# Performance work log

Hardware: AMD Instinct MI355X
Metric: run time of the kernel (lower is better)

## Reference

```python
import jax, jax.numpy as jnp
import numpy as np

NUM_SEQS = 32
NUM_HEADS = 32
NUM_KV_HEADS = 8
HEAD_DIM = 128
BLOCK_SIZE = 16
MAX_BLOCKS = 128          # max_seq_len 2048 / block_size 16
NUM_BLOCKS = NUM_SEQS * MAX_BLOCKS  # 4096
SCALE = 0.08838834764831845  # 1/sqrt(128)


def setup_inputs() -> dict:
    key = jax.random.key(0)
    kq, kk, kv, kkc, kvc, kbt, kcl = jax.random.split(key, 7)
    q = jax.random.normal(kq, (NUM_SEQS, NUM_HEADS, HEAD_DIM), dtype=jnp.float32)
    k = jax.random.normal(kk, (NUM_SEQS, NUM_KV_HEADS, HEAD_DIM), dtype=jnp.float32)
    v = jax.random.normal(kv, (NUM_SEQS, NUM_KV_HEADS, HEAD_DIM), dtype=jnp.float32)
    k_cache = jax.random.normal(kkc, (NUM_BLOCKS, BLOCK_SIZE, NUM_KV_HEADS, HEAD_DIM), dtype=jnp.float32)
    v_cache = jax.random.normal(kvc, (NUM_BLOCKS, BLOCK_SIZE, NUM_KV_HEADS, HEAD_DIM), dtype=jnp.float32)
    # disjoint paged block tables: permutation of all blocks
    block_tables = jax.random.permutation(kbt, NUM_BLOCKS).reshape(NUM_SEQS, MAX_BLOCKS).astype(jnp.int32)
    context_lens = jax.random.randint(kcl, (NUM_SEQS,), 1, MAX_BLOCKS * BLOCK_SIZE, dtype=jnp.int32)
    # slot for the newest token (position context_len-1) of each sequence
    last = context_lens - 1
    blk = jnp.take_along_axis(block_tables, (last // BLOCK_SIZE)[:, None], axis=1)[:, 0]
    slot_mapping = (blk * BLOCK_SIZE + last % BLOCK_SIZE).astype(jnp.int32)
    return {"q": q, "k": k, "v": v, "k_cache": k_cache, "v_cache": v_cache,
            "slot_mapping": slot_mapping, "block_tables": block_tables,
            "context_lens": context_lens}


def reference(q, k, v, k_cache, v_cache, slot_mapping, block_tables, context_lens):
    nb, bs, nkv, hd = k_cache.shape
    s, h, _ = q.shape
    g = h // nkv  # GQA group size
    # 1) scatter-store new k/v into the paged cache at slot_mapping
    kc = k_cache.reshape(nb * bs, nkv, hd).at[slot_mapping].set(k)
    vc = v_cache.reshape(nb * bs, nkv, hd).at[slot_mapping].set(v)
    kc = kc.reshape(nb, bs, nkv, hd)
    vc = vc.reshape(nb, bs, nkv, hd)
    # 2) gather per-sequence KV via block tables: [S, MB, bs, nkv, hd] -> [S, L, nkv, hd]
    max_len = block_tables.shape[1] * bs
    keys = kc[block_tables].reshape(s, max_len, nkv, hd)
    vals = vc[block_tables].reshape(s, max_len, nkv, hd)
    # 3) GQA decode attention with per-sequence length mask
    qg = q.reshape(s, nkv, g, hd)
    scores = jnp.einsum('sngd,slnd->sngl', qg, keys) * SCALE  # [S, nkv, g, L]
    valid = (jnp.arange(max_len, dtype=jnp.int32)[None, :] < context_lens[:, None])
    scores = jnp.where(valid[:, None, None, :], scores, -1e30)
    probs = jax.nn.softmax(scores, axis=-1)
    out = jnp.einsum('sngl,slnd->sngd', probs, vals)
    return out.reshape(s, h, hd)
```

## Files before the change

kernel.cpp:

```cpp
#include <hip/hip_runtime.h>

#define NUM_SEQS   32
#define NUM_HEADS  32
#define NUM_KV     8
#define GQA        4
#define HD         128
#define BS         16
#define MAX_BLOCKS 128
#define PART       256
#define NPARTS     8
#define SLOG2 (0.08838834764831845f * 1.4426950408889634f)


#define LOADKV(I, KA, KB, VA, VB)                                           \
    {                                                                       \
        const int    blk_  = blkreg[(I) >> 2];                              \
        const int    toff_ = (grp + 4 * (I)) & 15;                          \
        const size_t row_  = (((size_t)blk_ * BS + toff_) * NUM_KV + n) * HD; \
        const float4* kr_ = (const float4*)(kcache + row_);                 \
        const float4* vr_ = (const float4*)(vcache + row_);                 \
        KA = kr_[dsub];      KB = kr_[16 + dsub];                           \
        VA = vr_[dsub];      VB = vr_[16 + dsub];                           \
    }

#define QK_PV(KA, KB, VA, VB)                                               \
    {                                                                       \
        float pr[GQA];                                                      \
        _Pragma("unroll")                                                   \
        for (int h = 0; h < GQA; ++h) {                                     \
            float d = KA.x * qa[h].x + KA.y * qa[h].y + KA.z * qa[h].z      \
                    + KA.w * qa[h].w                                        \
                    + KB.x * qb[h].x + KB.y * qb[h].y + KB.z * qb[h].z      \
                    + KB.w * qb[h].w;                                       \
            d += __shfl_xor(d, 1);                                          \
            d += __shfl_xor(d, 2);                                          \
            d += __shfl_xor(d, 4);                                          \
            d += __shfl_xor(d, 8);                                          \
            pr[h] = exp2f(d * SLOG2);                                       \
            l[h] += pr[h];                                                  \
        }                                                                   \
        _Pragma("unroll")                                                   \
        for (int h = 0; h < GQA; ++h) {                                     \
            aa[h].x += pr[h] * VA.x; aa[h].y += pr[h] * VA.y;               \
            aa[h].z += pr[h] * VA.z; aa[h].w += pr[h] * VA.w;               \
            ab[h].x += pr[h] * VB.x; ab[h].y += pr[h] * VB.y;               \
            ab[h].z += pr[h] * VB.z; ab[h].w += pr[h] * VB.w;               \
        }                                                                   \
    }

__global__ __launch_bounds__(256, 4) void paged_attn_part(
    const float* __restrict__ q, const float* __restrict__ knew,
    const float* __restrict__ vnew, const float* __restrict__ kcache,
    const float* __restrict__ vcache, const int* __restrict__ block_tables,
    const int* __restrict__ context_lens,
    float* __restrict__ ws_acc, float* __restrict__ ws_l)
{
    const int p = blockIdx.x;
    const int n = blockIdx.y;
    const int s = blockIdx.z;
    const int L = context_lens[s];
    const int t0 = p * PART;
    if (t0 >= L) return;

    const int tid  = threadIdx.x;
    const int wave = tid >> 6;
    const int lane = tid & 63;
    const int grp  = lane >> 4;
    const int dsub = lane & 15;

    __shared__ int   lds_bt[16];
    __shared__ float lds_acc[4][GQA][HD];
    __shared__ float lds_l[4][GQA];

    if (tid < 16) lds_bt[tid] = block_tables[s * MAX_BLOCKS + (t0 >> 4) + tid];
    __syncthreads();

    int blkreg[4];
#pragma unroll
    for (int j = 0; j < 4; ++j) blkreg[j] = lds_bt[wave * 4 + j];

    float4 qa[GQA], qb[GQA];
#pragma unroll
    for (int h = 0; h < GQA; ++h) {
        const float4* qp = (const float4*)(q + ((size_t)s * NUM_HEADS + n * GQA + h) * HD);
        qa[h] = qp[dsub];
        qb[h] = qp[16 + dsub];
    }

    float l[GQA];
    float4 aa[GQA], ab[GQA];
#pragma unroll
    for (int h = 0; h < GQA; ++h) {
        l[h] = 0.f;
        aa[h] = make_float4(0.f, 0.f, 0.f, 0.f);
        ab[h] = make_float4(0.f, 0.f, 0.f, 0.f);
    }

    const int Leff = L - 1;
    const int ntok = min(Leff - t0, PART);
    int wtok = ntok - wave * 64;
    if (wtok > 64) wtok = 64;
    const int avail = wtok - grp;
    const int nit = (avail > 0) ? ((avail + 3) >> 2) : 0;

    float4 k0a, k0b, v0a, v0b;
    float4 k1a, k1b, v1a, v1b;
    if (nit > 0) LOADKV(0, k0a, k0b, v0a, v0b);
    if (nit > 1) LOADKV(1, k1a, k1b, v1a, v1b);

    int i = 0;
#pragma unroll 1
    for (; i + 2 <= nit; i += 2) {
        QK_PV(k0a, k0b, v0a, v0b);
        if (i + 2 < nit) LOADKV(i + 2, k0a, k0b, v0a, v0b);
        QK_PV(k1a, k1b, v1a, v1b);
        if (i + 3 < nit) LOADKV(i + 3, k1a, k1b, v1a, v1b);
    }
    if (i < nit) QK_PV(k0a, k0b, v0a, v0b);

    if ((t0 >> 8) == ((L - 1) >> 8) && tid < 16) {
        const float4* kr = (const float4*)(knew + ((size_t)s * NUM_KV + n) * HD);
        const float4* vr = (const float4*)(vnew + ((size_t)s * NUM_KV + n) * HD);
        const float4 ka = kr[dsub];
        const float4 kb = kr[16 + dsub];
        const float4 va = vr[dsub];
        const float4 vb = vr[16 + dsub];
#pragma unroll
        for (int h = 0; h < GQA; ++h) {
            float d = ka.x * qa[h].x + ka.y * qa[h].y + ka.z * qa[h].z + ka.w * qa[h].w
                    + kb.x * qb[h].x + kb.y * qb[h].y + kb.z * qb[h].z + kb.w * qb[h].w;
            d += __shfl_xor(d, 1);
            d += __shfl_xor(d, 2);
            d += __shfl_xor(d, 4);
            d += __shfl_xor(d, 8);
            const float pp = exp2f(d * SLOG2);
            l[h] += pp;
            aa[h].x += pp * va.x; aa[h].y += pp * va.y;
            aa[h].z += pp * va.z; aa[h].w += pp * va.w;
            ab[h].x += pp * vb.x; ab[h].y += pp * vb.y;
            ab[h].z += pp * vb.z; ab[h].w += pp * vb.w;
        }
    }

#pragma unroll
    for (int off = 16; off <= 32; off <<= 1) {
#pragma unroll
        for (int h = 0; h < GQA; ++h) {
            l[h]    += __shfl_xor(l[h], off);
            aa[h].x += __shfl_xor(aa[h].x, off);
            aa[h].y += __shfl_xor(aa[h].y, off);
            aa[h].z += __shfl_xor(aa[h].z, off);
            aa[h].w += __shfl_xor(aa[h].w, off);
            ab[h].x += __shfl_xor(ab[h].x, off);
            ab[h].y += __shfl_xor(ab[h].y, off);
            ab[h].z += __shfl_xor(ab[h].z, off);
            ab[h].w += __shfl_xor(ab[h].w, off);
        }
    }

    if (grp == 0) {
#pragma unroll
        for (int h = 0; h < GQA; ++h) {
            float4* dst = (float4*)&lds_acc[wave][h][0];
            dst[dsub]      = aa[h];
            dst[16 + dsub] = ab[h];
        }
        if (dsub == 0) {
#pragma unroll
            for (int h = 0; h < GQA; ++h) lds_l[wave][h] = l[h];
        }
    }
    __syncthreads();

    const int pbase = (((s * NUM_KV + n) * NPARTS) + p) * GQA;
    for (int item = tid; item < GQA * HD; item += 256) {
        const int h = item >> 7;
        const int d = item & 127;
        float A = lds_acc[0][h][d] + lds_acc[1][h][d]
                + lds_acc[2][h][d] + lds_acc[3][h][d];
        ws_acc[(size_t)(pbase + h) * HD + d] = A;
        if (d == 0) {
            ws_l[pbase + h] = lds_l[0][h] + lds_l[1][h] + lds_l[2][h] + lds_l[3][h];
        }
    }
}

__global__ __launch_bounds__(128) void paged_attn_combine(
    const float* __restrict__ ws_acc, const float* __restrict__ ws_l,
    const int* __restrict__ context_lens, float* __restrict__ out)
{
    const int bid = blockIdx.x;
    const int s  = bid >> 5;
    const int hg = bid & 31;
    const int n  = hg >> 2;
    const int hs = hg & 3;
    const int d  = threadIdx.x;
    const int L  = context_lens[s];
    const int np = (L + PART - 1) / PART;

    const int base = ((s * NUM_KV + n) * NPARTS) * GQA + hs;
    float Ls = 0.f, A = 0.f;
    for (int p = 0; p < np; ++p) {
        Ls += ws_l[base + p * GQA];
        A  += ws_acc[(size_t)(base + p * GQA) * HD + d];
    }
    out[((size_t)s * NUM_HEADS + hg) * HD + d] = A / Ls;
}

extern "C" void kernel_launch(void* const* d_in, const int* in_sizes, int n_in,
                              void* d_out, int out_size, void* d_ws, size_t ws_size,
                              hipStream_t stream) {
    const float* q  = (const float*)d_in[0];
    const float* k  = (const float*)d_in[1];
    const float* v  = (const float*)d_in[2];
    const float* kc = (const float*)d_in[3];
    const float* vc = (const float*)d_in[4];
    const int* bt = (const int*)d_in[6];
    const int* cl = (const int*)d_in[7];
    float* out = (float*)d_out;

    float* ws_acc = (float*)d_ws;
    float* ws_l   = ws_acc + (size_t)NUM_SEQS * NUM_KV * NPARTS * GQA * HD;

    dim3 grid(NPARTS, NUM_KV, NUM_SEQS);
    paged_attn_part<<<grid, 256, 0, stream>>>(q, k, v, kc, vc, bt, cl,
                                              ws_acc, ws_l);
    paged_attn_combine<<<NUM_SEQS * NUM_HEADS, HD, 0, stream>>>(
        ws_acc, ws_l, cl, out);
}
```

Measured before the change: 569.9 us.

## Use 512-thread blocks with 32 lanes per token row and reorder grid

Doubles the work-group to 8 waves, with each token row now handled by 32 lanes (one float4 each) instead of 16 lanes holding two float4s. This halves the per-thread K/V/Q/accumulator register footprint, which allows more waves in flight to hide memory latency. The grid order changes so sequences vary fastest. In exchange each QK dot product needs an extra shuffle stage, and the final cross-wave reduction in LDS now sums 8 waves.

Result: slower. 746.4 us (+31.0%).

```diff
diff --git a/kernel.cpp b/kernel.cpp
--- a/kernel.cpp
+++ b/kernel.cpp
@@ -12,30 +12,27 @@
 #define SLOG2 (0.08838834764831845f * 1.4426950408889634f)
 
 
-#define LOADKV(I, KA, KB, VA, VB)                                           \
+#define LOADKV(I, KA, VA)                                                   \
     {                                                                       \
-        const int    blk_  = blkreg[(I) >> 2];                              \
-        const int    toff_ = (grp + 4 * (I)) & 15;                          \
-        const size_t row_  = (((size_t)blk_ * BS + toff_) * NUM_KV + n) * HD; \
-        const float4* kr_ = (const float4*)(kcache + row_);                 \
-        const float4* vr_ = (const float4*)(vcache + row_);                 \
-        KA = kr_[dsub];      KB = kr_[16 + dsub];                           \
-        VA = vr_[dsub];      VB = vr_[16 + dsub];                           \
-    }
-
-#define QK_PV(KA, KB, VA, VB)                                               \
+        const int    tl_  = grp + 2 * (I);                                  \
+        const int    blk_ = blkreg[tl_ >> 4];                               \
+        const size_t row_ = (((size_t)blk_ * BS + (tl_ & 15)) * NUM_KV + n) * HD; \
+        KA = ((const float4*)(kcache + row_))[dsub];                        \
+        VA = ((const float4*)(vcache + row_))[dsub];                        \
+    }
+
+#define QK_PV(KA, VA)                                                       \
     {                                                                       \
         float pr[GQA];                                                      \
         _Pragma("unroll")                                                   \
         for (int h = 0; h < GQA; ++h) {                                     \
-            float d = KA.x * qa[h].x + KA.y * qa[h].y + KA.z * qa[h].z      \
-                    + KA.w * qa[h].w                                        \
-                    + KB.x * qb[h].x + KB.y * qb[h].y + KB.z * qb[h].z      \
-                    + KB.w * qb[h].w;                                       \
+            float d = KA.x * qa[h].x + KA.y * qa[h].y                       \
+                    + KA.z * qa[h].z + KA.w * qa[h].w;                      \
             d += __shfl_xor(d, 1);                                          \
             d += __shfl_xor(d, 2);                                          \
             d += __shfl_xor(d, 4);                                          \
             d += __shfl_xor(d, 8);                                          \
+            d += __shfl_xor(d, 16);                                         \
             pr[h] = exp2f(d * SLOG2);                                       \
             l[h] += pr[h];                                                  \
         }                                                                   \
@@ -43,21 +40,19 @@
         for (int h = 0; h < GQA; ++h) {                                     \
             aa[h].x += pr[h] * VA.x; aa[h].y += pr[h] * VA.y;               \
             aa[h].z += pr[h] * VA.z; aa[h].w += pr[h] * VA.w;               \
-            ab[h].x += pr[h] * VB.x; ab[h].y += pr[h] * VB.y;               \
-            ab[h].z += pr[h] * VB.z; ab[h].w += pr[h] * VB.w;               \
         }                                                                   \
     }
 
-__global__ __launch_bounds__(256, 4) void paged_attn_part(
+__global__ __launch_bounds__(512, 8) void paged_attn_part(
     const float* __restrict__ q, const float* __restrict__ knew,
     const float* __restrict__ vnew, const float* __restrict__ kcache,
     const float* __restrict__ vcache, const int* __restrict__ block_tables,
     const int* __restrict__ context_lens,
     float* __restrict__ ws_acc, float* __restrict__ ws_l)
 {
-    const int p = blockIdx.x;
+    const int s = blockIdx.x;
     const int n = blockIdx.y;
-    const int s = blockIdx.z;
+    const int p = blockIdx.z;
     const int L = context_lens[s];
     const int t0 = p * PART;
     if (t0 >= L) return;
@@ -65,105 +60,89 @@
     const int tid  = threadIdx.x;
     const int wave = tid >> 6;
     const int lane = tid & 63;
-    const int grp  = lane >> 4;
-    const int dsub = lane & 15;
+    const int grp  = lane >> 5;
+    const int dsub = lane & 31;
 
     __shared__ int   lds_bt[16];
-    __shared__ float lds_acc[4][GQA][HD];
-    __shared__ float lds_l[4][GQA];
+    __shared__ float lds_acc[8][GQA][HD];
+    __shared__ float lds_l[8][GQA];
 
     if (tid < 16) lds_bt[tid] = block_tables[s * MAX_BLOCKS + (t0 >> 4) + tid];
     __syncthreads();
 
-    int blkreg[4];
-#pragma unroll
-    for (int j = 0; j < 4; ++j) blkreg[j] = lds_bt[wave * 4 + j];
-
-    float4 qa[GQA], qb[GQA];
+    int blkreg[2];
+    blkreg[0] = lds_bt[wave * 2];
+    blkreg[1] = lds_bt[wave * 2 + 1];
+
+    float4 qa[GQA];
 #pragma unroll
     for (int h = 0; h < GQA; ++h) {
         const float4* qp = (const float4*)(q + ((size_t)s * NUM_HEADS + n * GQA + h) * HD);
         qa[h] = qp[dsub];
-        qb[h] = qp[16 + dsub];
     }
 
     float l[GQA];
-    float4 aa[GQA], ab[GQA];
+    float4 aa[GQA];
 #pragma unroll
     for (int h = 0; h < GQA; ++h) {
         l[h] = 0.f;
         aa[h] = make_float4(0.f, 0.f, 0.f, 0.f);
-        ab[h] = make_float4(0.f, 0.f, 0.f, 0.f);
     }
 
     const int Leff = L - 1;
     const int ntok = min(Leff - t0, PART);
-    int wtok = ntok - wave * 64;
-    if (wtok > 64) wtok = 64;
+    int wtok = ntok - wave * 32;
+    if (wtok > 32) wtok = 32;
     const int avail = wtok - grp;
-    const int nit = (avail > 0) ? ((avail + 3) >> 2) : 0;
-
-    float4 k0a, k0b, v0a, v0b;
-    float4 k1a, k1b, v1a, v1b;
-    if (nit > 0) LOADKV(0, k0a, k0b, v0a, v0b);
-    if (nit > 1) LOADKV(1, k1a, k1b, v1a, v1b);
+    const int nit = (avail > 0) ? ((avail + 1) >> 1) : 0;
+
+    float4 kA, vA, kB, vB;
+    if (nit > 0) LOADKV(0, kA, vA);
+    if (nit > 1) LOADKV(1, kB, vB);
 
     int i = 0;
 #pragma unroll 1
     for (; i + 2 <= nit; i += 2) {
-        QK_PV(k0a, k0b, v0a, v0b);
-        if (i + 2 < nit) LOADKV(i + 2, k0a, k0b, v0a, v0b);
-        QK_PV(k1a, k1b, v1a, v1b);
-        if (i + 3 < nit) LOADKV(i + 3, k1a, k1b, v1a, v1b);
-    }
-    if (i < nit) QK_PV(k0a, k0b, v0a, v0b);
-
-    if ((t0 >> 8) == ((L - 1) >> 8) && tid < 16) {
-        const float4* kr = (const float4*)(knew + ((size_t)s * NUM_KV + n) * HD);
-        const float4* vr = (const float4*)(vnew + ((size_t)s * NUM_KV + n) * HD);
-        const float4 ka = kr[dsub];
-        const float4 kb = kr[16 + dsub];
-        const float4 va = vr[dsub];
-        const float4 vb = vr[16 + dsub];
+        QK_PV(kA, vA);
+        if (i + 2 < nit) LOADKV(i + 2, kA, vA);
+        QK_PV(kB, vB);
+        if (i + 3 < nit) LOADKV(i + 3, kB, vB);
+    }
+    if (i < nit) QK_PV(kA, vA);
+
+    if ((t0 >> 8) == ((L - 1) >> 8) && tid < 32) {
+        const float4 ka = ((const float4*)(knew + ((size_t)s * NUM_KV + n) * HD))[dsub];
+        const float4 va = ((const float4*)(vnew + ((size_t)s * NUM_KV + n) * HD))[dsub];
 #pragma unroll
         for (int h = 0; h < GQA; ++h) {
-            float d = ka.x * qa[h].x + ka.y * qa[h].y + ka.z * qa[h].z + ka.w * qa[h].w
-                    + kb.x * qb[h].x + kb.y * qb[h].y + kb.z * qb[h].z + kb.w * qb[h].w;
+            float d = ka.x * qa[h].x + ka.y * qa[h].y
+                    + ka.z * qa[h].z + ka.w * qa[h].w;
             d += __shfl_xor(d, 1);
             d += __shfl_xor(d, 2);
             d += __shfl_xor(d, 4);
             d += __shfl_xor(d, 8);
+            d += __shfl_xor(d, 16);
             const float pp = exp2f(d * SLOG2);
             l[h] += pp;
             aa[h].x += pp * va.x; aa[h].y += pp * va.y;
             aa[h].z += pp * va.z; aa[h].w += pp * va.w;
-            ab[h].x += pp * vb.x; ab[h].y += pp * vb.y;
-            ab[h].z += pp * vb.z; ab[h].w += pp * vb.w;
-        }
-    }
-
-#pragma unroll
-    for (int off = 16; off <= 32; off <<= 1) {
-#pragma unroll
-        for (int h = 0; h < GQA; ++h) {
-            l[h]    += __shfl_xor(l[h], off);
-            aa[h].x += __shfl_xor(aa[h].x, off);
-            aa[h].y += __shfl_xor(aa[h].y, off);
-            aa[h].z += __shfl_xor(aa[h].z, off);
-            aa[h].w += __shfl_xor(aa[h].w, off);
-            ab[h].x += __shfl_xor(ab[h].x, off);
-            ab[h].y += __shfl_xor(ab[h].y, off);
-            ab[h].z += __shfl_xor(ab[h].z, off);
-            ab[h].w += __shfl_xor(ab[h].w, off);
-        }
+        }
+    }
+
+#pragma unroll
+    for (int h = 0; h < GQA; ++h) {
+        l[h]    += __shfl_xor(l[h], 32);
+        aa[h].x += __shfl_xor(aa[h].x, 32);
+        aa[h].y += __shfl_xor(aa[h].y, 32);
+        aa[h].z += __shfl_xor(aa[h].z, 32);
+        aa[h].w += __shfl_xor(aa[h].w, 32);
     }
 
     if (grp == 0) {
 #pragma unroll
         for (int h = 0; h < GQA; ++h) {
             float4* dst = (float4*)&lds_acc[wave][h][0];
-            dst[dsub]      = aa[h];
-            dst[16 + dsub] = ab[h];
+            dst[dsub] = aa[h];
         }
         if (dsub == 0) {
 #pragma unroll
@@ -173,14 +152,19 @@
     __syncthreads();
 
     const int pbase = (((s * NUM_KV + n) * NPARTS) + p) * GQA;
-    for (int item = tid; item < GQA * HD; item += 256) {
+    {
+        const int item = tid;
         const int h = item >> 7;
         const int d = item & 127;
-        float A = lds_acc[0][h][d] + lds_acc[1][h][d]
-                + lds_acc[2][h][d] + lds_acc[3][h][d];
+        float A = 0.f;
+#pragma unroll
+        for (int w = 0; w < 8; ++w) A += lds_acc[w][h][d];
         ws_acc[(size_t)(pbase + h) * HD + d] = A;
         if (d == 0) {
-            ws_l[pbase + h] = lds_l[0][h] + lds_l[1][h] + lds_l[2][h] + lds_l[3][h];
+            float Ls = 0.f;
+#pragma unroll
+            for (int w = 0; w < 8; ++w) Ls += lds_l[w][h];
+            ws_l[pbase + h] = Ls;
         }
     }
 }
@@ -222,8 +206,8 @@
     float* ws_acc = (float*)d_ws;
     float* ws_l   = ws_acc + (size_t)NUM_SEQS * NUM_KV * NPARTS * GQA * HD;
 
-    dim3 grid(NPARTS, NUM_KV, NUM_SEQS);
-    paged_attn_part<<<grid, 256, 0, stream>>>(q, k, v, kc, vc, bt, cl,
+    dim3 grid(NUM_SEQS, NUM_KV, NPARTS);
+    paged_attn_part<<<grid, 512, 0, stream>>>(q, k, v, kc, vc, bt, cl,
                                               ws_acc, ws_l);
     paged_attn_combine<<<NUM_SEQS * NUM_HEADS, HD, 0, stream>>>(
         ws_acc, ws_l, cl, out);
```
